# Optimization experiments

Hardware: AMD Instinct MI355X
Metric: run time of the kernel (lower is better)

Reference implementation:

```python
import jax, jax.numpy as jnp
import numpy as np


def _gelu(x):
    # tf.nn.gelu default is exact (non-approximate)
    return jax.nn.gelu(x, approximate=False)


def _conv1d_same(x, w, b, stride):
    # x: [B, T, Cin], w: [K, Cin, Cout] -> [B, T', Cout], TF 'SAME' padding
    y = jax.lax.conv_general_dilated(
        x, w, window_strides=(stride,), padding='SAME',
        dimension_numbers=('NWC', 'WIO', 'NWC'))
    return y + b


def _pos_encoding(seq_len, d_model, dtype):
    pos = jnp.arange(seq_len, dtype=jnp.float32)[:, None]
    i = jnp.arange(d_model)[None, :]
    angle = pos / jnp.power(10000.0, (2 * (i // 2)).astype(jnp.float32) / d_model)
    pe = jnp.where(i % 2 == 0, jnp.sin(angle), jnp.cos(angle))
    return pe.astype(dtype)  # [seq_len, d_model]


def _lstm(x, Wk, Wr, b):
    # x: [B, S, F]; Keras gate order i, f, g(c), o. Inference: dropout is no-op.
    B = x.shape[0]
    H = Wr.shape[0]

    def step(carry, xt):
        h, c = carry
        z = xt @ Wk + h @ Wr + b  # [B, 4H]
        i, f, g, o = jnp.split(z, 4, axis=-1)
        c = jax.nn.sigmoid(f) * c + jax.nn.sigmoid(i) * jnp.tanh(g)
        h = jax.nn.sigmoid(o) * jnp.tanh(c)
        return (h, c), h

    h0 = jnp.zeros((B, H), x.dtype)
    (_, _), hs = jax.lax.scan(step, (h0, h0), jnp.swapaxes(x, 0, 1))
    return jnp.swapaxes(hs, 0, 1)  # [B, S, H]


def setup_inputs() -> dict:
    key = jax.random.key(0)
    ks = jax.random.split(key, 8)
    B, T, Cin = 8, 2000, 128
    D = 512
    x = jax.random.normal(ks[0], (B, T, Cin), dtype=jnp.float32)
    conv1_w = jax.random.normal(ks[1], (3, Cin, 4096), dtype=jnp.float32) * 0.02
    conv1_b = jnp.zeros((4096,), dtype=jnp.float32)
    conv2_w = jax.random.normal(ks[2], (3, 4096, 1024), dtype=jnp.float32) * 0.02
    conv2_b = jnp.zeros((1024,), dtype=jnp.float32)
    Fin = T // 2  # LSTM feature dim after stride-2 conv + permute
    lstm_k = jax.random.normal(ks[3], (Fin, 4 * D), dtype=jnp.float32) * 0.02
    lstm_r = jax.random.normal(ks[4], (D, 4 * D), dtype=jnp.float32) * 0.02
    lstm_b = jnp.zeros((4 * D,), dtype=jnp.float32).at[D:2 * D].set(1.0)  # unit_forget_bias
    return dict(x=x, conv1_w=conv1_w, conv1_b=conv1_b, conv2_w=conv2_w,
                conv2_b=conv2_b, lstm_k=lstm_k, lstm_r=lstm_r, lstm_b=lstm_b)


def reference(x, conv1_w, conv1_b, conv2_w, conv2_b, lstm_k, lstm_r, lstm_b):
    h = _gelu(_conv1d_same(x, conv1_w, conv1_b, 1))      # [B, T, 4096]
    h = _gelu(_conv1d_same(h, conv2_w, conv2_b, 2))      # [B, T/2, 1024]
    h = jnp.transpose(h, (0, 2, 1))                      # [B, 1024, T/2]
    out = _lstm(h, lstm_k, lstm_r, lstm_b)               # [B, 1024, D]
    pe = _pos_encoding(out.shape[1], out.shape[2], out.dtype)
    return out + pe[None, :, :]
```

## Files before the change

kernel.cpp:

```cpp
#include <hip/hip_runtime.h>
#include <cmath>
#include <cstdint>

typedef __bf16 bf16;
typedef __bf16 bf16x8 __attribute__((ext_vector_type(8)));
typedef unsigned short u16x8 __attribute__((ext_vector_type(8)));
typedef float f32x4 __attribute__((ext_vector_type(4)));
typedef unsigned u32x4 __attribute__((ext_vector_type(4)));

#define HPOISON 0x7FC07FC0u

static __device__ __forceinline__ float gelu_exact(float x) {
    return 0.5f * x * (1.f + erff(x * 0.70710678118654752f));
}

static __device__ __forceinline__ float fast_sigmoid(float x) {
    return __builtin_amdgcn_rcpf(1.f + __expf(-x));
}
static __device__ __forceinline__ float fast_tanh(float x) {
    return 1.f - 2.f * __builtin_amdgcn_rcpf(1.f + __expf(2.f * x));
}

static __device__ __forceinline__ void store16u_sc1(unsigned* p, u32x4 v) {
    asm volatile("global_store_dwordx4 %0, %1, off sc1" :: "v"(p), "v"(v) : "memory");
}
static __device__ __forceinline__ void load64u_sc1(const unsigned* p, u32x4& a, u32x4& b,
                                                   u32x4& c, u32x4& d) {
    asm volatile(
        "global_load_dwordx4 %0, %4, off sc1\n\t"
        "global_load_dwordx4 %1, %4, off offset:16 sc1\n\t"
        "global_load_dwordx4 %2, %4, off offset:32 sc1\n\t"
        "global_load_dwordx4 %3, %4, off offset:48 sc1\n\t"
        "s_waitcnt vmcnt(0)"
        : "=&v"(a), "=&v"(b), "=&v"(c), "=&v"(d)
        : "v"(p) : "memory");
}

__global__ void cvt_xpad_kernel(const float* __restrict__ x, bf16* __restrict__ xp) {
    int idx = blockIdx.x * 256 + threadIdx.x;
    if (idx >= 8 * 2002 * 128) return;
    int c = idx & 127;
    int rest = idx >> 7;
    int tp = rest % 2002;
    int b = rest / 2002;
    float v = 0.f;
    if (tp >= 1 && tp <= 2000) v = x[(b * 2000 + tp - 1) * 128 + c];
    xp[idx] = (bf16)v;
}

template <typename OT>
__global__ void transpose_cvt_kernel(const float* __restrict__ in, OT* __restrict__ out,
                                     int R, int C, int Rpad) {
    __shared__ float tile[32][33];
    int tx = threadIdx.x & 31, ty = threadIdx.x >> 5;
    int r0 = blockIdx.y * 32, c0 = blockIdx.x * 32;
    for (int i = ty; i < 32; i += 8) {
        int r = r0 + i, c = c0 + tx;
        tile[i][tx] = (r < R && c < C) ? in[(size_t)r * C + c] : 0.f;
    }
    __syncthreads();
    for (int i = ty; i < 32; i += 8) {
        int c = c0 + i, r = r0 + tx;
        if (c < C && r < Rpad) out[(size_t)c * Rpad + r] = (OT)tile[tx][i];
    }
}

__global__ void transpose_split_kernel(const float* __restrict__ in, bf16* __restrict__ hi,
                                       bf16* __restrict__ lo, int R, int C) {
    __shared__ float tile[32][33];
    int tx = threadIdx.x & 31, ty = threadIdx.x >> 5;
    int r0 = blockIdx.y * 32, c0 = blockIdx.x * 32;
    for (int i = ty; i < 32; i += 8) {
        int r = r0 + i, c = c0 + tx;
        tile[i][tx] = (r < R && c < C) ? in[(size_t)r * C + c] : 0.f;
    }
    __syncthreads();
    for (int i = ty; i < 32; i += 8) {
        int c = c0 + i, r = r0 + tx;
        if (c < C && r < R) {
            float v = tile[tx][i];
            bf16 h = (bf16)v;
            size_t o = (size_t)c * R + r;
            hi[o] = h;
            lo[o] = (bf16)(v - (float)h);
        }
    }
}

__global__ void zero_aux_kernel(bf16* __restrict__ h1) {
    int idx = blockIdx.x * 256 + threadIdx.x;
    if (idx < 8 * 4096) {
        int b = idx >> 12, n = idx & 4095;
        h1[((size_t)(b * 2001 + 2000)) * 4096 + n] = (bf16)0.f;
    }
}

__global__ void poison_kernel(unsigned* __restrict__ hstep) {
    size_t i = (size_t)blockIdx.x * 256 + threadIdx.x;
    if (i < (size_t)1024 * 4096 / 4) {
        u32x4 pz = {HPOISON, HPOISON, HPOISON, HPOISON};
        *(u32x4*)(hstep + i * 4) = pz;
    }
}

template <int MODE>
__launch_bounds__(256)
__global__ void gemm_kernel(const bf16* __restrict__ A, const bf16* __restrict__ BT,
                            const float* __restrict__ bias, void* __restrict__ Cout) {
    constexpr int KTOT = (MODE == 0) ? 384 : (MODE == 1) ? 12288 : 1024;
    constexpr int MTOT = (MODE == 0) ? 16000 : (MODE == 1) ? 8000 : 8192;
    __shared__ __align__(16) bf16 As[128 * 32];
    __shared__ __align__(16) bf16 Bs[128 * 32];
    const int tid = threadIdx.x;
    const int lane = tid & 63, wave = tid >> 6;
    const int m0 = blockIdx.y * 128, n0 = blockIdx.x * 128;
    const int wm = (wave >> 1) * 64, wn = (wave & 1) * 64;

    f32x4 acc[4][4];
#pragma unroll
    for (int mi = 0; mi < 4; ++mi)
#pragma unroll
        for (int ni = 0; ni < 4; ++ni) acc[mi][ni] = (f32x4){0.f, 0.f, 0.f, 0.f};

    for (int kt = 0; kt < KTOT / 32; ++kt) {
        const int k0 = kt * 32;
        __syncthreads();
#pragma unroll
        for (int s = 0; s < 2; ++s) {
            int ch = tid + s * 256;
            int row = ch >> 2;
            int ko = (ch & 3) * 8;
            int m = m0 + row;
            if (m > MTOT - 1) m = MTOT - 1;
            const bf16* ga;
            if (MODE == 0) {
                int b = m / 2000, t = m - b * 2000;
                ga = A + ((size_t)(b * 2002 + t + (k0 >> 7)) * 128 + (k0 & 127) + ko);
            } else if (MODE == 1) {
                int b = m / 1000, t = m - b * 1000;
                ga = A + ((size_t)(b * 2001 + 2 * t + (k0 >> 12)) * 4096 + (k0 & 4095) + ko);
            } else {
                ga = A + ((size_t)m * 1000 + k0 + ko);
            }
            *(uint4*)&As[ch * 8] = *(const uint4*)ga;
            const bf16* gb = BT + ((size_t)(n0 + row) * KTOT + k0 + ko);
            *(uint4*)&Bs[ch * 8] = *(const uint4*)gb;
        }
        __syncthreads();
        bf16x8 af[4], bfr[4];
#pragma unroll
        for (int i = 0; i < 4; ++i)
            af[i] = *(const bf16x8*)&As[(wm + i * 16 + (lane & 15)) * 32 + (lane >> 4) * 8];
#pragma unroll
        for (int i = 0; i < 4; ++i)
            bfr[i] = *(const bf16x8*)&Bs[(wn + i * 16 + (lane & 15)) * 32 + (lane >> 4) * 8];
#pragma unroll
        for (int mi = 0; mi < 4; ++mi)
#pragma unroll
            for (int ni = 0; ni < 4; ++ni)
                acc[mi][ni] = __builtin_amdgcn_mfma_f32_16x16x32_bf16(af[mi], bfr[ni], acc[mi][ni], 0, 0, 0);
    }

#pragma unroll
    for (int mi = 0; mi < 4; ++mi) {
        int rb = m0 + wm + mi * 16 + (lane >> 4) * 4;
#pragma unroll
        for (int ni = 0; ni < 4; ++ni) {
            int col = n0 + wn + ni * 16 + (lane & 15);
#pragma unroll
            for (int i = 0; i < 4; ++i) {
                int row = rb + i;
                float v = acc[mi][ni][i];
                if (MODE == 0) {
                    float y = gelu_exact(v + bias[col]);
                    int b = row / 2000, t = row - b * 2000;
                    ((bf16*)Cout)[(size_t)(b * 2001 + t) * 4096 + col] = (bf16)y;
                } else if (MODE == 1) {
                    if (row < 8000) {
                        float y = gelu_exact(v + bias[col]);
                        int b = row / 1000, t = row - b * 1000;
                        ((bf16*)Cout)[(size_t)(b * 1024 + col) * 1000 + t] = (bf16)y;
                    }
                } else {
                    ((float*)Cout)[(size_t)row * 2048 + col] = v + bias[col];
                }
            }
        }
    }
}

__launch_bounds__(256, 1)
__global__ void lstm_persist_kernel(const float* __restrict__ Zin,
                                    const bf16* __restrict__ WrHi,
                                    const bf16* __restrict__ WrLo,
                                    unsigned* __restrict__ hstep,
                                    float* __restrict__ out) {
    __shared__ __align__(16) unsigned char hS[2][8192];
    __shared__ float zex[4][128];
    const int tid = threadIdx.x;
    const int wv = tid >> 6;
    const int w = blockIdx.x;
    const int lane = tid & 63;

    bf16x8 bh[16], bl[16];
    {
        const size_t cb = (size_t)(wv * 512 + w * 16 + (lane & 15)) * 512 + (lane >> 4) * 8;
#pragma unroll
        for (int kk = 0; kk < 16; ++kk) {
            bh[kk] = *(const bf16x8*)&WrHi[cb + kk * 32];
            bl[kk] = *(const bf16x8*)&WrLo[cb + kk * 32];
        }
    }

    const int b = tid >> 4, u = tid & 15, j = w * 16 + u;
    float c_state = 0.f;
    float zin0 = 0.f, zin1 = 0.f, zin2 = 0.f, zin3 = 0.f;
    const float invf = powf(10000.f, -(float)(2 * (j >> 1)) * (1.f / 512.f));
    if (tid < 128) {
        const float* zp = Zin + (size_t)(b * 1024) * 2048;
        zin0 = zp[j]; zin1 = zp[512 + j]; zin2 = zp[1024 + j]; zin3 = zp[1536 + j];
    }

    const int rowsel = lane & 15;
    const int kq = lane >> 4;
    const unsigned aswz = (unsigned)((rowsel & 7) << 4);
    const unsigned abase = (unsigned)((rowsel & 7) * 1024);

    const int srow = tid >> 5;
    const int scol = tid & 31;
    const unsigned ssw = (unsigned)((srow & 7) << 4);
    const unsigned sbase = (unsigned)(srow * 1024);

    for (int t = 0; t < 1024; ++t) {
        {
            unsigned vv[16];
            if (t > 0) {
                const unsigned* src = hstep + (size_t)t * 4096 + srow * 512 + scol * 16;
                for (;;) {
                    u32x4 qa, qb, qc, qd;
                    load64u_sc1(src, qa, qb, qc, qd);
#pragma unroll
                    for (int i = 0; i < 4; ++i) {
                        vv[i] = qa[i]; vv[4 + i] = qb[i]; vv[8 + i] = qc[i]; vv[12 + i] = qd[i];
                    }
                    bool ok = true;
#pragma unroll
                    for (int i = 0; i < 16; ++i) ok = ok && (vv[i] != HPOISON);
                    if (ok) break;
                    __builtin_amdgcn_s_sleep(1);
                }
            } else {
#pragma unroll
                for (int i = 0; i < 16; ++i) vv[i] = 0u;
            }
            u16x8 h0, h1v, l0, l1v;
#pragma unroll
            for (int i = 0; i < 8; ++i) {
                h0[i]  = (unsigned short)(vv[i] >> 16);
                l0[i]  = (unsigned short)(vv[i] & 0xFFFFu);
                h1v[i] = (unsigned short)(vv[8 + i] >> 16);
                l1v[i] = (unsigned short)(vv[8 + i] & 0xFFFFu);
            }
            unsigned o0 = (unsigned)(scol * 32);
            *(u16x8*)&hS[0][sbase + (o0 ^ ssw)] = h0;
            *(u16x8*)&hS[0][sbase + ((o0 + 16) ^ ssw)] = h1v;
            *(u16x8*)&hS[1][sbase + (o0 ^ ssw)] = l0;
            *(u16x8*)&hS[1][sbase + ((o0 + 16) ^ ssw)] = l1v;
        }
        __syncthreads();
        f32x4 acc0 = {0.f, 0.f, 0.f, 0.f}, acc1 = {0.f, 0.f, 0.f, 0.f}, acc2 = {0.f, 0.f, 0.f, 0.f};
#pragma unroll
        for (int kk = 0; kk < 16; ++kk) {
            unsigned ko = (unsigned)((kk * 4 + kq) * 16);
            bf16x8 ah = *(const bf16x8*)&hS[0][abase + (ko ^ aswz)];
            bf16x8 al = *(const bf16x8*)&hS[1][abase + (ko ^ aswz)];
            acc0 = __builtin_amdgcn_mfma_f32_16x16x32_bf16(ah, bh[kk], acc0, 0, 0, 0);
            acc1 = __builtin_amdgcn_mfma_f32_16x16x32_bf16(al, bh[kk], acc1, 0, 0, 0);
            acc2 = __builtin_amdgcn_mfma_f32_16x16x32_bf16(ah, bl[kk], acc2, 0, 0, 0);
        }
        if (kq < 2) {
#pragma unroll
            for (int i = 0; i < 4; ++i)
                zex[wv][(kq * 4 + i) * 16 + rowsel] = acc0[i] + acc1[i] + acc2[i];
        }
        __syncthreads();
        if (tid < 128) {
            float zi = zex[0][tid] + zin0;
            float zf = zex[1][tid] + zin1;
            float zg = zex[2][tid] + zin2;
            float zo = zex[3][tid] + zin3;
            float ig = fast_sigmoid(zi);
            float fg = fast_sigmoid(zf);
            float og = fast_sigmoid(zo);
            float c = fg * c_state + ig * fast_tanh(zg);
            c_state = c;
            float hval = og * fast_tanh(c);
            if (t < 1023) {
                bf16 hh = (bf16)hval;
                bf16 hlo = (bf16)(hval - (float)hh);
                unsigned pk = ((unsigned)*(unsigned short*)&hh << 16) |
                              (unsigned)*(unsigned short*)&hlo;
                unsigned p1 = (unsigned)__shfl_down((int)pk, 1);
                unsigned p2 = (unsigned)__shfl_down((int)pk, 2);
                unsigned p3 = (unsigned)__shfl_down((int)pk, 3);
                if ((tid & 3) == 0) {
                    u32x4 hv = {pk, p1, p2, p3};
                    store16u_sc1(hstep + (size_t)(t + 1) * 4096 + b * 512 + j, hv);
                }
            }
            float ang = (float)t * invf;
            float pe = (j & 1) ? cosf(ang) : sinf(ang);
            out[(size_t)(b * 1024 + t) * 512 + j] = hval + pe;
            if (t < 1023) {
                const float* zp = Zin + (size_t)(b * 1024 + t + 1) * 2048;
                zin0 = zp[j]; zin1 = zp[512 + j]; zin2 = zp[1024 + j]; zin3 = zp[1536 + j];
            }
        }
    }
}

extern "C" void kernel_launch(void* const* d_in, const int* in_sizes, int n_in,
                              void* d_out, int out_size, void* d_ws, size_t ws_size,
                              hipStream_t stream) {
    const float* x  = (const float*)d_in[0];
    const float* w1 = (const float*)d_in[1];
    const float* b1 = (const float*)d_in[2];
    const float* w2 = (const float*)d_in[3];
    const float* b2 = (const float*)d_in[4];
    const float* wk = (const float*)d_in[5];
    const float* wr = (const float*)d_in[6];
    const float* lb = (const float*)d_in[7];
    float* out = (float*)d_out;

    uint8_t* ws = (uint8_t*)d_ws;
    size_t off = 0;
    auto alloc = [&](size_t bytes) {
        void* p = ws + off;
        off += (bytes + 255) & ~(size_t)255;
        return p;
    };
    bf16* xpad = (bf16*)alloc((size_t)8 * 2002 * 128 * 2);
    bf16* W1T  = (bf16*)alloc((size_t)4096 * 384 * 2);
    bf16* W2T  = (bf16*)alloc((size_t)1024 * 12288 * 2);
    bf16* WkT  = (bf16*)alloc((size_t)2048 * 1024 * 2);
    bf16* WrHi = (bf16*)alloc((size_t)2048 * 512 * 2);
    bf16* WrLo = (bf16*)alloc((size_t)2048 * 512 * 2);
    bf16* h1   = (bf16*)alloc((size_t)8 * 2001 * 4096 * 2);
    bf16* h2T  = (bf16*)alloc((size_t)8 * 1024 * 1000 * 2 + 256);
    float* Zin = (float*)alloc((size_t)8 * 1024 * 2048 * 4);
    unsigned* hstep = (unsigned*)h1;

    cvt_xpad_kernel<<<(8 * 2002 * 128 + 255) / 256, 256, 0, stream>>>(x, xpad);
    transpose_cvt_kernel<bf16><<<dim3(128, 12), 256, 0, stream>>>(w1, W1T, 384, 4096, 384);
    transpose_cvt_kernel<bf16><<<dim3(32, 384), 256, 0, stream>>>(w2, W2T, 12288, 1024, 12288);
    transpose_cvt_kernel<bf16><<<dim3(64, 32), 256, 0, stream>>>(wk, WkT, 1000, 2048, 1024);
    transpose_split_kernel<<<dim3(64, 16), 256, 0, stream>>>(wr, WrHi, WrLo, 512, 2048);
    zero_aux_kernel<<<(8 * 4096 + 255) / 256, 256, 0, stream>>>(h1);

    gemm_kernel<0><<<dim3(32, 125), 256, 0, stream>>>(xpad, W1T, b1, (void*)h1);
    gemm_kernel<1><<<dim3(8, 63), 256, 0, stream>>>(h1, W2T, b2, (void*)h2T);
    poison_kernel<<<4096, 256, 0, stream>>>(hstep);
    gemm_kernel<2><<<dim3(16, 64), 256, 0, stream>>>(h2T, WkT, lb, (void*)Zin);

    lstm_persist_kernel<<<32, 256, 0, stream>>>(Zin, WrHi, WrLo, hstep, out);
}
```

Before: 3.257 ms.

## Offload LSTM output writes round-robin and use direct global-to-LDS GEMM loads

In the GEMM, the A/B tile staging now uses global_load_lds (direct global-to-LDS copy), which avoids passing the data through registers. In the persistent LSTM kernel, each block no longer writes its own slice of out every step. Instead, one block per step, chosen round-robin, rebuilds the whole previous h from the bf16 hi/lo pair it already loaded and writes the full row with positional encoding. The Zin load moves to after the barrier and a shared table of inverse frequencies is added. The goal is to take the per-step sin/cos and scattered store work off the critical serial path. The cost is that the stored h is the hi+lo bf16 reconstruction, a small precision change, and the writing block does extra work on that step.

After: 3.702 ms. 1.14x slower.

```diff
diff --git a/kernel.cpp b/kernel.cpp
--- a/kernel.cpp
+++ b/kernel.cpp
@@ -34,6 +34,16 @@
         "s_waitcnt vmcnt(0)"
         : "=&v"(a), "=&v"(b), "=&v"(c), "=&v"(d)
         : "v"(p) : "memory");
+}
+
+static __device__ __forceinline__ void gl_lds16(const bf16* g, bf16* l) {
+#if defined(__has_builtin) && __has_builtin(__builtin_amdgcn_global_load_lds)
+    __builtin_amdgcn_global_load_lds(
+        (const unsigned __attribute__((address_space(1)))*)g,
+        (unsigned __attribute__((address_space(3)))*)l, 16, 0, 0);
+#else
+    *(uint4*)l = *(const uint4*)g;
+#endif
 }
 
 __global__ void cvt_xpad_kernel(const float* __restrict__ x, bf16* __restrict__ xp) {
@@ -142,9 +152,9 @@
             } else {
                 ga = A + ((size_t)m * 1000 + k0 + ko);
             }
-            *(uint4*)&As[ch * 8] = *(const uint4*)ga;
+            gl_lds16(ga, &As[ch * 8]);
             const bf16* gb = BT + ((size_t)(n0 + row) * KTOT + k0 + ko);
-            *(uint4*)&Bs[ch * 8] = *(const uint4*)gb;
+            gl_lds16(gb, &Bs[ch * 8]);
         }
         __syncthreads();
         bf16x8 af[4], bfr[4];
@@ -197,6 +207,7 @@
                                     float* __restrict__ out) {
     __shared__ __align__(16) unsigned char hS[2][8192];
     __shared__ float zex[4][128];
+    __shared__ float invfS[512];
     const int tid = threadIdx.x;
     const int wv = tid >> 6;
     const int w = blockIdx.x;
@@ -211,15 +222,12 @@
             bl[kk] = *(const bf16x8*)&WrLo[cb + kk * 32];
         }
     }
+    for (int i = tid; i < 512; i += 256)
+        invfS[i] = powf(10000.f, -(float)(2 * (i >> 1)) * (1.f / 512.f));
+    __syncthreads();
 
     const int b = tid >> 4, u = tid & 15, j = w * 16 + u;
     float c_state = 0.f;
-    float zin0 = 0.f, zin1 = 0.f, zin2 = 0.f, zin3 = 0.f;
-    const float invf = powf(10000.f, -(float)(2 * (j >> 1)) * (1.f / 512.f));
-    if (tid < 128) {
-        const float* zp = Zin + (size_t)(b * 1024) * 2048;
-        zin0 = zp[j]; zin1 = zp[512 + j]; zin2 = zp[1024 + j]; zin3 = zp[1536 + j];
-    }
 
     const int rowsel = lane & 15;
     const int kq = lane >> 4;
@@ -230,6 +238,8 @@
     const int scol = tid & 31;
     const unsigned ssw = (unsigned)((srow & 7) << 4);
     const unsigned sbase = (unsigned)(srow * 1024);
+
+    unsigned keep[16];
 
     for (int t = 0; t < 1024; ++t) {
         {
@@ -253,6 +263,8 @@
 #pragma unroll
                 for (int i = 0; i < 16; ++i) vv[i] = 0u;
             }
+#pragma unroll
+            for (int i = 0; i < 16; ++i) keep[i] = vv[i];
             u16x8 h0, h1v, l0, l1v;
 #pragma unroll
             for (int i = 0; i < 8; ++i) {
@@ -268,6 +280,11 @@
             *(u16x8*)&hS[1][sbase + ((o0 + 16) ^ ssw)] = l1v;
         }
         __syncthreads();
+        float zin0 = 0.f, zin1 = 0.f, zin2 = 0.f, zin3 = 0.f;
+        if (tid < 128) {
+            const float* zp = Zin + (size_t)(b * 1024 + t) * 2048;
+            zin0 = zp[j]; zin1 = zp[512 + j]; zin2 = zp[1024 + j]; zin3 = zp[1536 + j];
+        }
         f32x4 acc0 = {0.f, 0.f, 0.f, 0.f}, acc1 = {0.f, 0.f, 0.f, 0.f}, acc2 = {0.f, 0.f, 0.f, 0.f};
 #pragma unroll
         for (int kk = 0; kk < 16; ++kk) {
@@ -307,14 +324,29 @@
                     u32x4 hv = {pk, p1, p2, p3};
                     store16u_sc1(hstep + (size_t)(t + 1) * 4096 + b * 512 + j, hv);
                 }
-            }
-            float ang = (float)t * invf;
-            float pe = (j & 1) ? cosf(ang) : sinf(ang);
-            out[(size_t)(b * 1024 + t) * 512 + j] = hval + pe;
-            if (t < 1023) {
-                const float* zp = Zin + (size_t)(b * 1024 + t + 1) * 2048;
-                zin0 = zp[j]; zin1 = zp[512 + j]; zin2 = zp[1024 + j]; zin3 = zp[1536 + j];
-            }
+            } else {
+                float ang = 1023.f * invfS[j];
+                float pe = (j & 1) ? cosf(ang) : sinf(ang);
+                out[(size_t)(b * 1024 + 1023) * 512 + j] = hval + pe;
+            }
+        }
+        if (t > 0 && w == (t & 31)) {
+            const float ts = (float)(t - 1);
+            float ovals[16];
+#pragma unroll
+            for (int i = 0; i < 16; ++i) {
+                float hi = __uint_as_float(keep[i] & 0xFFFF0000u);
+                float lo = __uint_as_float(keep[i] << 16);
+                int jj = scol * 16 + i;
+                float ang = ts * invfS[jj];
+                float pe = (jj & 1) ? cosf(ang) : sinf(ang);
+                ovals[i] = hi + lo + pe;
+            }
+            float* op = out + ((size_t)(srow * 1024) + (t - 1)) * 512 + scol * 16;
+#pragma unroll
+            for (int q = 0; q < 4; ++q)
+                *(f32x4*)(op + q * 4) =
+                    (f32x4){ovals[4 * q], ovals[4 * q + 1], ovals[4 * q + 2], ovals[4 * q + 3]};
         }
     }
 }
```

## Use direct global-to-LDS loads in GEMM and split conv2 transposed store

Applied to the files above, without the earlier changes.

GEMM tile loads now use the global_load_lds builtin, which writes global data straight into shared memory instead of staging it through registers. The conv2 GEMM epilogue also writes its output in natural row-major order into a scratch buffer that aliases Zin, and a separate tiled transpose kernel then produces the [B,1024,T] layout. This is meant to replace the strided, uncoalesced scattered stores with coalesced ones, at the cost of an extra kernel and an extra pass over memory. Direct LDS loads may require specific LDS address alignment and wave-uniform base addressing; the per-lane LDS addresses used here may not match what the builtin expects, which risks incorrect data.

Result: no change. 3.228 ms (median of 2 runs) (-0.9%).

```diff
diff --git a/kernel.cpp b/kernel.cpp
--- a/kernel.cpp
+++ b/kernel.cpp
@@ -36,6 +36,16 @@
         : "v"(p) : "memory");
 }
 
+static __device__ __forceinline__ void gl_lds16(const bf16* g, bf16* l) {
+#if defined(__has_builtin) && __has_builtin(__builtin_amdgcn_global_load_lds)
+    __builtin_amdgcn_global_load_lds(
+        (const unsigned __attribute__((address_space(1)))*)g,
+        (unsigned __attribute__((address_space(3)))*)l, 16, 0, 0);
+#else
+    *(uint4*)l = *(const uint4*)g;
+#endif
+}
+
 __global__ void cvt_xpad_kernel(const float* __restrict__ x, bf16* __restrict__ xp) {
     int idx = blockIdx.x * 256 + threadIdx.x;
     if (idx >= 8 * 2002 * 128) return;
@@ -84,6 +94,22 @@
             hi[o] = h;
             lo[o] = (bf16)(v - (float)h);
         }
+    }
+}
+
+__global__ void transpose_h2_kernel(const bf16* __restrict__ in, bf16* __restrict__ out) {
+    __shared__ bf16 tile[32][33];
+    int tx = threadIdx.x & 31, ty = threadIdx.x >> 5;
+    int b = blockIdx.z;
+    int t0 = blockIdx.x * 32, n0 = blockIdx.y * 32;
+    for (int i = ty; i < 32; i += 8) {
+        int t = t0 + i;
+        tile[i][tx] = (t < 1000) ? in[((size_t)(b * 1000 + t)) * 1024 + n0 + tx] : (bf16)0.f;
+    }
+    __syncthreads();
+    for (int i = ty; i < 32; i += 8) {
+        int n = n0 + i, t = t0 + tx;
+        if (t < 1000) out[((size_t)(b * 1024 + n)) * 1000 + t] = tile[tx][i];
     }
 }
 
@@ -142,9 +168,9 @@
             } else {
                 ga = A + ((size_t)m * 1000 + k0 + ko);
             }
-            *(uint4*)&As[ch * 8] = *(const uint4*)ga;
+            gl_lds16(ga, &As[ch * 8]);
             const bf16* gb = BT + ((size_t)(n0 + row) * KTOT + k0 + ko);
-            *(uint4*)&Bs[ch * 8] = *(const uint4*)gb;
+            gl_lds16(gb, &Bs[ch * 8]);
         }
         __syncthreads();
         bf16x8 af[4], bfr[4];
@@ -178,8 +204,7 @@
                 } else if (MODE == 1) {
                     if (row < 8000) {
                         float y = gelu_exact(v + bias[col]);
-                        int b = row / 1000, t = row - b * 1000;
-                        ((bf16*)Cout)[(size_t)(b * 1024 + col) * 1000 + t] = (bf16)y;
+                        ((bf16*)Cout)[(size_t)row * 1024 + col] = (bf16)y;
                     }
                 } else {
                     ((float*)Cout)[(size_t)row * 2048 + col] = v + bias[col];
@@ -349,6 +374,7 @@
     bf16* h2T  = (bf16*)alloc((size_t)8 * 1024 * 1000 * 2 + 256);
     float* Zin = (float*)alloc((size_t)8 * 1024 * 2048 * 4);
     unsigned* hstep = (unsigned*)h1;
+    bf16* h2nat = (bf16*)Zin;
 
     cvt_xpad_kernel<<<(8 * 2002 * 128 + 255) / 256, 256, 0, stream>>>(x, xpad);
     transpose_cvt_kernel<bf16><<<dim3(128, 12), 256, 0, stream>>>(w1, W1T, 384, 4096, 384);
@@ -358,7 +384,8 @@
     zero_aux_kernel<<<(8 * 4096 + 255) / 256, 256, 0, stream>>>(h1);
 
     gemm_kernel<0><<<dim3(32, 125), 256, 0, stream>>>(xpad, W1T, b1, (void*)h1);
-    gemm_kernel<1><<<dim3(8, 63), 256, 0, stream>>>(h1, W2T, b2, (void*)h2T);
+    gemm_kernel<1><<<dim3(8, 63), 256, 0, stream>>>(h1, W2T, b2, (void*)h2nat);
+    transpose_h2_kernel<<<dim3(32, 32, 8), 256, 0, stream>>>(h2nat, h2T);
     poison_kernel<<<4096, 256, 0, stream>>>(hstep);
     gemm_kernel<2><<<dim3(16, 64), 256, 0, stream>>>(h2T, WkT, lb, (void*)Zin);
 
```
